# Performance work log

Measured on AMD Instinct MI355X. Metric: run time of the kernel, lower is better.

## Reference

```python
import jax, jax.numpy as jnp
import numpy as np

N_LAYER, N_HEAD, D_MODEL, D_K, D_HIDDEN = 8, 8, 512, 64, 2048
N_CONTEXT, N_DICT, MAG = 1024, 8192, 0.05
B, T = 8, 1024


def _sinusoidal_pos(n_context, d_model):
    i2 = np.arange(0, d_model, 2)
    inv = 1.0 / (10000.0 ** (i2 / d_model))
    ang = np.arange(n_context, dtype=np.float32)[:, None] * inv[None, :]
    pe = np.zeros((1, n_context, d_model), np.float32)
    pe[0, :, 0::2] = np.sin(ang)
    pe[0, :, 1::2] = np.cos(ang)
    return jnp.asarray(pe)


def setup_inputs() -> dict:
    key = jax.random.key(0)
    ks = jax.random.split(key, 10)
    p = lambda k, *s: jax.random.normal(k, s, jnp.float32) * MAG
    return {
        "x": jax.random.randint(ks[0], (B, T), 0, N_DICT),
        "last_only": False,
        "capture_stats": False,
        "embedding": p(ks[1], N_DICT, D_MODEL),
        "pos_embedding": _sinusoidal_pos(N_CONTEXT, D_MODEL),  # fixedpos='True', not trained
        "wq": p(ks[2], N_LAYER, N_HEAD, D_MODEL, D_K),
        "wk": p(ks[3], N_LAYER, N_HEAD, D_MODEL, D_K),
        "wv": p(ks[4], N_LAYER, N_HEAD, D_MODEL, D_MODEL),
        "mlp0": p(ks[5], N_LAYER, D_MODEL, D_HIDDEN),
        "mlpb": p(ks[6], N_LAYER, 1, D_HIDDEN),
        "mlp1": p(ks[7], N_LAYER, D_HIDDEN, D_MODEL),
        "unembedding": p(ks[8], D_MODEL, N_DICT),
        "bias": p(ks[9], 1, 1, N_DICT),
    }


def _ln(x):
    # torch LayerNorm(elementwise_affine=False, bias=False), eps=1e-5, biased var
    mu = jnp.mean(x, axis=-1, keepdims=True)
    var = jnp.mean((x - mu) ** 2, axis=-1, keepdims=True)
    return (x - mu) * jax.lax.rsqrt(var + 1e-5)


def reference(x, last_only, capture_stats, embedding, pos_embedding,
              wq, wk, wv, mlp0, mlpb, mlp1, unembedding, bias):
    del capture_stats  # stats path disabled (capture_stats=False)
    t = x.shape[1]
    h = embedding[x] + pos_embedding[:, :t, :]   # [B,T,M]
    h = _ln(h)                                    # enorm='True', lmul = 1/ldiv = 1
    mask = jnp.tril(jnp.ones((t, t), dtype=bool))

    def layer(h, params):
        wq_l, wk_l, wv_l, m0, mb, m1 = params
        q = jnp.einsum('btm,hmq->bhtq', h, wq_l)
        k = jnp.einsum('bom,hmk->bhok', h, wk_l)
        v = jnp.einsum('bom,hmv->bhov', h, wv_l)
        attn = jnp.einsum('bhtq,bhoq->bhto', q, k)
        # exp(clamp(.,max=50)) then tril then sum-normalize (NOT softmax)
        attn = jnp.where(mask, jnp.exp(jnp.minimum(attn, 50.0)), 0.0)
        attn = attn / (jnp.sum(attn, axis=-1, keepdims=True) + 1e-10)
        vsum = jnp.einsum('bhto,bhov->btv', attn, v)  # sums over heads
        h = _ln(h + vsum)                              # amul = 1, lmul = 1
        y = jax.nn.relu(jnp.einsum('btm,mh->bth', h, m0) + mb)
        y = jnp.einsum('bth,hm->btm', y, m1)
        h = _ln(h + y)                                 # pmul = 1, lmul = 1
        return h, None

    h, _ = jax.lax.scan(layer, h, (wq, wk, wv, mlp0, mlpb, mlp1))
    if last_only:
        h = h[:, -1:, :]
    return jnp.einsum('btm,md->btd', h, unembedding) + bias
```

## Files before the change

kernel.cpp:

```cpp
#include <hip/hip_runtime.h>
#include <hip/hip_bf16.h>

#define BB 8
#define TT 1024
#define DM 512
#define NH 8
#define DK 64
#define DH 2048
#define NL 8
#define ND 8192

typedef __attribute__((ext_vector_type(8))) short short8v;
typedef __attribute__((ext_vector_type(8))) _Float16 f16x8;
typedef __attribute__((ext_vector_type(4))) float f32x4;
typedef __attribute__((ext_vector_type(4))) unsigned short ushort4v;
typedef unsigned short u16;

#define MFMA16(a, b, c) __builtin_amdgcn_mfma_f32_16x16x32_bf16(a, b, c, 0, 0, 0)
#define MFMAH(a, b, c)  __builtin_amdgcn_mfma_f32_16x16x32_f16(a, b, c, 0, 0, 0)

__device__ __forceinline__ u16 bf16_bits(float f) {
  union { __hip_bfloat16 h; u16 u; } cv;
  cv.h = __float2bfloat16(f);
  return cv.u;
}
__device__ __forceinline__ float bits_to_f32(u16 u) {
  union { __hip_bfloat16 h; u16 u; } cv;
  cv.u = u;
  return __bfloat162float(cv.h);
}

__device__ __forceinline__ void gload16(const void* g, void* l) {
  __builtin_amdgcn_global_load_lds(
      (const __attribute__((address_space(1))) unsigned int*)g,
      (__attribute__((address_space(3))) unsigned int*)l, 16, 0, 0);
}

#define WAITVM(N) asm volatile("s_waitcnt vmcnt(" #N ")" ::: "memory")
#define BAR() { __builtin_amdgcn_s_barrier(); asm volatile("" ::: "memory"); }

__device__ __forceinline__ void block_reduce2(float& a, float& b) {
  #pragma unroll
  for (int off = 32; off > 0; off >>= 1) {
    a += __shfl_down(a, off, 64);
    b += __shfl_down(b, off, 64);
  }
  __shared__ float sa[4], sb[4];
  int w = threadIdx.x >> 6;
  if ((threadIdx.x & 63) == 0) { sa[w] = a; sb[w] = b; }
  __syncthreads();
  if (threadIdx.x == 0) {
    sa[0] = sa[0] + sa[1] + sa[2] + sa[3];
    sb[0] = sb[0] + sb[1] + sb[2] + sb[3];
  }
  __syncthreads();
  a = sa[0]; b = sb[0];
}

__device__ __forceinline__ void store_hilo(u16* hh, u16* hl, size_t i, float v) {
  u16 hb = bf16_bits(v);
  hh[i] = hb;
  hl[i] = bf16_bits(v - bits_to_f32(hb));
}

__global__ __launch_bounds__(256) void embed_ln_kernel(
    const int* __restrict__ x, const float* __restrict__ emb,
    const float* __restrict__ pos, float* __restrict__ h,
    u16* __restrict__ hh, u16* __restrict__ hl) {
  int bt = blockIdx.x;
  int t = bt & (TT - 1);
  int tid = threadIdx.x;
  int row = x[bt];
  float v0 = emb[(size_t)row * DM + tid]       + pos[(size_t)t * DM + tid];
  float v1 = emb[(size_t)row * DM + tid + 256] + pos[(size_t)t * DM + tid + 256];
  float s = v0 + v1, sq = v0 * v0 + v1 * v1;
  block_reduce2(s, sq);
  float mu  = s * (1.0f / DM);
  float var = sq * (1.0f / DM) - mu * mu;
  float rs  = rsqrtf(var + 1e-5f);
  float r0 = (v0 - mu) * rs, r1 = (v1 - mu) * rs;
  h[(size_t)bt * DM + tid] = r0;
  h[(size_t)bt * DM + tid + 256] = r1;
  store_hilo(hh, hl, (size_t)bt * DM + tid, r0);
  store_hilo(hh, hl, (size_t)bt * DM + tid + 256, r1);
}

template<bool BF16ADD>
__global__ __launch_bounds__(256) void ln_residual_kernel(
    float* __restrict__ h, const void* __restrict__ add_, int rowStride, int nsum,
    u16* __restrict__ hh, u16* __restrict__ hl) {
  int bt = blockIdx.x;
  int tid = threadIdx.x;
  size_t base = (size_t)bt * (size_t)rowStride;
  float v0 = h[(size_t)bt * DM + tid];
  float v1 = h[(size_t)bt * DM + tid + 256];
  if (BF16ADD) {
    const u16* add = (const u16*)add_;
    for (int i = 0; i < nsum; ++i) {
      v0 += bits_to_f32(add[base + (size_t)i * DM + tid]);
      v1 += bits_to_f32(add[base + (size_t)i * DM + tid + 256]);
    }
  } else {
    const float* add = (const float*)add_;
    for (int i = 0; i < nsum; ++i) {
      v0 += add[base + (size_t)i * DM + tid];
      v1 += add[base + (size_t)i * DM + tid + 256];
    }
  }
  float s = v0 + v1, sq = v0 * v0 + v1 * v1;
  block_reduce2(s, sq);
  float mu  = s * (1.0f / DM);
  float var = sq * (1.0f / DM) - mu * mu;
  float rs  = rsqrtf(var + 1e-5f);
  float r0 = (v0 - mu) * rs, r1 = (v1 - mu) * rs;
  h[(size_t)bt * DM + tid] = r0;
  h[(size_t)bt * DM + tid + 256] = r1;
  store_hilo(hh, hl, (size_t)bt * DM + tid, r0);
  store_hilo(hh, hl, (size_t)bt * DM + tid + 256, r1);
}

__device__ __forceinline__ void tconv_body(
    const float* __restrict__ in, u16* __restrict__ oh, u16* __restrict__ ol,
    int K, int Nb, bool hilo, float (*T)[65]) {
  int tid = threadIdx.x;
  int k0 = blockIdx.x * 64, n0 = blockIdx.y * 64;
  int g = n0 / Nb;
  const float* src = in + (size_t)g * K * Nb + (n0 - g * Nb);
  #pragma unroll
  for (int rep = 0; rep < 16; ++rep) {
    int idx = rep * 256 + tid;
    int i = idx >> 6, j = idx & 63;
    T[i][j] = src[(size_t)(k0 + i) * Nb + j];
  }
  __syncthreads();
  #pragma unroll
  for (int rep = 0; rep < 16; ++rep) {
    int idx = rep * 256 + tid;
    int j = idx >> 6, i = idx & 63;
    float v = T[i][j];
    size_t oa = (size_t)(n0 + j) * K + k0 + i;
    u16 hb = bf16_bits(v);
    oh[oa] = hb;
    if (hilo) ol[oa] = bf16_bits(v - bits_to_f32(hb));
  }
}

__global__ __launch_bounds__(256) void transpose_layer(
    const float* __restrict__ wq, const float* __restrict__ wk,
    const float* __restrict__ wv, const float* __restrict__ w0,
    const float* __restrict__ w1,
    u16* qh, u16* ql, u16* kh, u16* kl, u16* vT, u16* t0, u16* t1) {
  __shared__ float T[64][65];
  int z = blockIdx.z;
  const float* in;
  u16 *oh, *ol = nullptr;
  int K, Nb, gx, gy;
  bool hilo = false;
  switch (z) {
    case 0: in = wq; oh = qh; ol = ql; K = 512;  Nb = 64;   gx = 8;  gy = 8;  hilo = true; break;
    case 1: in = wk; oh = kh; ol = kl; K = 512;  Nb = 64;   gx = 8;  gy = 8;  hilo = true; break;
    case 2: in = wv; oh = vT;          K = 512;  Nb = 512;  gx = 8;  gy = 64; break;
    case 3: in = w0; oh = t0;          K = 512;  Nb = 2048; gx = 8;  gy = 32; break;
    default: in = w1; oh = t1;         K = 2048; Nb = 512;  gx = 32; gy = 8;  break;
  }
  if ((int)blockIdx.x >= gx || (int)blockIdx.y >= gy) return;
  tconv_body(in, oh, ol, K, Nb, hilo, T);
}

__global__ __launch_bounds__(256) void transpose_ue(
    const float* __restrict__ ue, u16* __restrict__ ueT) {
  __shared__ float T[64][65];
  tconv_body(ue, ueT, nullptr, 512, 8192, false, T);
}

template<int MODE>
__global__ __launch_bounds__(256, 2) void gemm_mfma(
    const u16* __restrict__ A, const u16* __restrict__ Bt,
    const float* __restrict__ bias, void* __restrict__ Oo,
    int M, int N, int K) {
  __shared__ u16 As[2][8192];
  __shared__ u16 Bs[2][8192];
  int tid = threadIdx.x;
  int lane = tid & 63, w = tid >> 6;
  int l15 = lane & 15, g = lane >> 4;
  int m0 = blockIdx.x * 128, n0 = blockIdx.y * 128;
  int wr = w >> 1, wc = w & 1;
  int nt = K >> 6;

  f32x4 acc[4][4];
  #pragma unroll
  for (int i = 0; i < 4; ++i)
    #pragma unroll
    for (int j = 0; j < 4; ++j)
      #pragma unroll
      for (int r = 0; r < 4; ++r) acc[i][j][r] = 0.f;

  auto stage = [&](int t, int buf) {
    int k0 = t << 6;
    #pragma unroll
    for (int j = 0; j < 4; ++j) {
      int idx = j * 256 + tid;
      int row = idx >> 3, cs = (idx & 7) ^ (row & 7);
      gload16(A + (size_t)(m0 + row) * K + k0 + cs * 8, &As[buf][idx * 8]);
    }
    #pragma unroll
    for (int j = 0; j < 4; ++j) {
      int idx = j * 256 + tid;
      int row = idx >> 3, cs = (idx & 7) ^ (row & 7);
      gload16(Bt + (size_t)(n0 + row) * K + k0 + cs * 8, &Bs[buf][idx * 8]);
    }
  };

  stage(0, 0);
  for (int t = 0; t < nt; ++t) {
    int cur = t & 1;
    if (t + 1 < nt) {
      stage(t + 1, cur ^ 1);
      WAITVM(8);
    } else {
      WAITVM(0);
    }
    BAR();
    short8v af[4][2], bf[4][2];
    #pragma unroll
    for (int mi = 0; mi < 4; ++mi) {
      int row = wr * 64 + mi * 16 + l15;
      #pragma unroll
      for (int ks = 0; ks < 2; ++ks) {
        int ch = (ks * 4 + g) ^ (row & 7);
        af[mi][ks] = *(const short8v*)&As[cur][row * 64 + ch * 8];
      }
    }
    #pragma unroll
    for (int ni = 0; ni < 4; ++ni) {
      int row = wc * 64 + ni * 16 + l15;
      #pragma unroll
      for (int ks = 0; ks < 2; ++ks) {
        int ch = (ks * 4 + g) ^ (row & 7);
        bf[ni][ks] = *(const short8v*)&Bs[cur][row * 64 + ch * 8];
      }
    }
    #pragma unroll
    for (int mi = 0; mi < 4; ++mi)
      #pragma unroll
      for (int ni = 0; ni < 4; ++ni) {
        acc[mi][ni] = MFMA16(af[mi][0], bf[ni][0], acc[mi][ni]);
        acc[mi][ni] = MFMA16(af[mi][1], bf[ni][1], acc[mi][ni]);
      }
    BAR();
  }

  #pragma unroll
  for (int mi = 0; mi < 4; ++mi) {
    #pragma unroll
    for (int ni = 0; ni < 4; ++ni) {
      int mrow = m0 + wr * 64 + mi * 16 + g * 4;
      int ncol = n0 + wc * 64 + ni * 16 + l15;
      if (MODE == 0) {
        int head = ncol >> 9, dv = ncol & (DM - 1);
        int bb = mrow >> 10, t0 = mrow & (TT - 1);
        ushort4v pk;
        #pragma unroll
        for (int r = 0; r < 4; ++r) pk[r] = bf16_bits(acc[mi][ni][r]);
        *(ushort4v*)((u16*)Oo + ((((size_t)bb * NH + head) * DM + dv) << 10) + t0) = pk;
      } else if (MODE == 1) {
        float bv = bias[ncol];
        #pragma unroll
        for (int r = 0; r < 4; ++r)
          ((u16*)Oo)[(size_t)(mrow + r) * N + ncol] =
              bf16_bits(fmaxf(acc[mi][ni][r] + bv, 0.f));
      } else if (MODE == 2) {
        #pragma unroll
        for (int r = 0; r < 4; ++r)
          ((float*)Oo)[(size_t)(mrow + r) * N + ncol] = acc[mi][ni][r];
      } else {
        float bv = bias[ncol];
        #pragma unroll
        for (int r = 0; r < 4; ++r)
          ((float*)Oo)[(size_t)(mrow + r) * N + ncol] = acc[mi][ni][r] + bv;
      }
    }
  }
}

__global__ __launch_bounds__(256, 2) void gemm_qk(
    const u16* __restrict__ Ah, const u16* __restrict__ Al,
    const u16* __restrict__ Bh, const u16* __restrict__ Bl,
    _Float16* __restrict__ Oq, int K) {
  __shared__ u16 As[2][8192];
  __shared__ u16 Bs[2][8192];
  int tid = threadIdx.x;
  int lane = tid & 63, w = tid >> 6;
  int l15 = lane & 15, g = lane >> 4;
  int m0 = blockIdx.x * 128, n0 = blockIdx.y * 128;
  int wr = w >> 1, wc = w & 1;
  int nt = K >> 5;

  f32x4 acc[4][4];
  #pragma unroll
  for (int i = 0; i < 4; ++i)
    #pragma unroll
    for (int j = 0; j < 4; ++j)
      #pragma unroll
      for (int r = 0; r < 4; ++r) acc[i][j][r] = 0.f;

  auto stage = [&](int t, int buf) {
    int k0 = t << 5;
    #pragma unroll
    for (int j = 0; j < 4; ++j) {
      int idx = j * 256 + tid;
      int row = idx >> 3, cs = (idx & 7) ^ (row & 7);
      const u16* src = (cs < 4) ? Ah : Al;
      gload16(src + (size_t)(m0 + row) * K + k0 + (cs & 3) * 8, &As[buf][idx * 8]);
    }
    #pragma unroll
    for (int j = 0; j < 4; ++j) {
      int idx = j * 256 + tid;
      int row = idx >> 3, cs = (idx & 7) ^ (row & 7);
      const u16* src = (cs < 4) ? Bh : Bl;
      gload16(src + (size_t)(n0 + row) * K + k0 + (cs & 3) * 8, &Bs[buf][idx * 8]);
    }
  };

  stage(0, 0);
  for (int t = 0; t < nt; ++t) {
    int cur = t & 1;
    if (t + 1 < nt) {
      stage(t + 1, cur ^ 1);
      WAITVM(8);
    } else {
      WAITVM(0);
    }
    BAR();
    short8v ah[4], al[4], bh[4], bl[4];
    #pragma unroll
    for (int mi = 0; mi < 4; ++mi) {
      int row = wr * 64 + mi * 16 + l15;
      ah[mi] = *(const short8v*)&As[cur][row * 64 + (g ^ (row & 7)) * 8];
      al[mi] = *(const short8v*)&As[cur][row * 64 + ((g + 4) ^ (row & 7)) * 8];
    }
    #pragma unroll
    for (int ni = 0; ni < 4; ++ni) {
      int row = wc * 64 + ni * 16 + l15;
      bh[ni] = *(const short8v*)&Bs[cur][row * 64 + (g ^ (row & 7)) * 8];
      bl[ni] = *(const short8v*)&Bs[cur][row * 64 + ((g + 4) ^ (row & 7)) * 8];
    }
    #pragma unroll
    for (int mi = 0; mi < 4; ++mi)
      #pragma unroll
      for (int ni = 0; ni < 4; ++ni) {
        acc[mi][ni] = MFMA16(ah[mi], bh[ni], acc[mi][ni]);
        acc[mi][ni] = MFMA16(al[mi], bh[ni], acc[mi][ni]);
        acc[mi][ni] = MFMA16(ah[mi], bl[ni], acc[mi][ni]);
      }
    BAR();
  }

  #pragma unroll
  for (int mi = 0; mi < 4; ++mi) {
    #pragma unroll
    for (int ni = 0; ni < 4; ++ni) {
      int mrow = m0 + wr * 64 + mi * 16 + g * 4;
      int ncol = n0 + wc * 64 + ni * 16 + l15;
      int head = ncol >> 6, dk = ncol & (DK - 1);
      int bb = mrow >> 10;
      #pragma unroll
      for (int r = 0; r < 4; ++r) {
        int t = (mrow + r) & (TT - 1);
        size_t ad = (((size_t)bb * NH + head) * TT + t) * DK + dk;
        Oq[ad] = (_Float16)acc[mi][ni][r];
      }
    }
  }
}

__global__ __launch_bounds__(256, 2) void attn_mfma_kernel(
    const _Float16* __restrict__ qp, const _Float16* __restrict__ kp,
    const __hip_bfloat16* __restrict__ vt_, u16* __restrict__ o) {
  __shared__ __align__(16) u16 Pl[2][64 * 64];
  __shared__ float rs_lds[64];

  const u16* vtp = (const u16*)vt_;

  int tid = threadIdx.x;
  int lane = tid & 63;
  int w = tid >> 6;
  int l15 = lane & 15, g = lane >> 4;
  int blk = blockIdx.x;
  int bh = blk & 63;
  int tt = 15 - (blk >> 6);

  if (tid < 64) rs_lds[tid] = 0.f;

  size_t qbase = (((size_t)bh * TT) + tt * 64 + w * 16 + l15) * DK + g * 8;
  f16x8 qf[2];
  qf[0] = *(const f16x8*)(qp + qbase);
  qf[1] = *(const f16x8*)(qp + qbase + 32);

  f32x4 oacc[4][8];
  #pragma unroll
  for (int qt = 0; qt < 4; ++qt)
    #pragma unroll
    for (int dv = 0; dv < 8; ++dv)
      #pragma unroll
      for (int r = 0; r < 4; ++r) oacc[qt][dv][r] = 0.f;

  __syncthreads();

  for (int ot = 0; ot <= tt; ++ot) {
    int ob = ot * 64;
    bool diag = (ot == tt);
    int buf = ot & 1;
    size_t kbase = (((size_t)bh * TT) + ob + l15) * DK + g * 8;
    f16x8 kf[4][2];
    #pragma unroll
    for (int ct = 0; ct < 4; ++ct) {
      kf[ct][0] = *(const f16x8*)(kp + kbase + (size_t)ct * 16 * DK);
      kf[ct][1] = *(const f16x8*)(kp + kbase + (size_t)ct * 16 * DK + 32);
    }
    f32x4 sacc[4];
    #pragma unroll
    for (int ct = 0; ct < 4; ++ct)
      #pragma unroll
      for (int r = 0; r < 4; ++r) sacc[ct][r] = 0.f;
    #pragma unroll
    for (int ct = 0; ct < 4; ++ct)
      #pragma unroll
      for (int ks = 0; ks < 2; ++ks)
        sacc[ct] = MFMAH(qf[ks], kf[ct][ks], sacc[ct]);
    size_t vbase = ((size_t)bh * DM + w * 128 + l15) * TT + ob + g * 8;
    short8v vf0[8];
    #pragma unroll
    for (int dv = 0; dv < 8; ++dv)
      vf0[dv] = *(const short8v*)(vtp + vbase + (size_t)dv * 16 * TT);
    float psum[4] = {0.f, 0.f, 0.f, 0.f};
    #pragma unroll
    for (int ct = 0; ct < 4; ++ct) {
      #pragma unroll
      for (int r = 0; r < 4; ++r) {
        float s = sacc[ct][r];
        float p = __expf(fminf(s, 50.f));
        if (diag && (ct * 16 + l15 > w * 16 + g * 4 + r)) p = 0.f;
        psum[r] += p;
        int q = w * 16 + g * 4 + r;
        int byte = (q * 128 + (ct * 16 + l15) * 2) ^ ((q & 7) << 4);
        *(u16*)((char*)Pl[buf] + byte) = bf16_bits(p);
      }
    }
    #pragma unroll
    for (int r = 0; r < 4; ++r) {
      float v = psum[r];
      v += __shfl_xor(v, 1, 16);
      v += __shfl_xor(v, 2, 16);
      v += __shfl_xor(v, 4, 16);
      v += __shfl_xor(v, 8, 16);
      if (l15 == 0) rs_lds[w * 16 + g * 4 + r] += v;
    }
    __syncthreads();
    short8v vf1[8];
    #pragma unroll
    for (int dv = 0; dv < 8; ++dv)
      vf1[dv] = *(const short8v*)(vtp + vbase + 32 + (size_t)dv * 16 * TT);
    short8v pf[4];
    #pragma unroll
    for (int qt = 0; qt < 4; ++qt) {
      int q = qt * 16 + l15;
      int byte = (q * 128 + g * 16) ^ ((q & 7) << 4);
      pf[qt] = *(short8v*)((char*)Pl[buf] + byte);
    }
    #pragma unroll
    for (int dv = 0; dv < 8; ++dv)
      #pragma unroll
      for (int qt = 0; qt < 4; ++qt)
        oacc[qt][dv] = MFMA16(pf[qt], vf0[dv], oacc[qt][dv]);
    #pragma unroll
    for (int qt = 0; qt < 4; ++qt) {
      int q = qt * 16 + l15;
      int byte = (q * 128 + 64 + g * 16) ^ ((q & 7) << 4);
      pf[qt] = *(short8v*)((char*)Pl[buf] + byte);
    }
    #pragma unroll
    for (int dv = 0; dv < 8; ++dv)
      #pragma unroll
      for (int qt = 0; qt < 4; ++qt)
        oacc[qt][dv] = MFMA16(pf[qt], vf1[dv], oacc[qt][dv]);
  }
  __syncthreads();
  int b = bh >> 3, hh2 = bh & 7;
  #pragma unroll
  for (int qt = 0; qt < 4; ++qt) {
    #pragma unroll
    for (int r = 0; r < 4; ++r) {
      int q = qt * 16 + g * 4 + r;
      float rs = 1.0f / (rs_lds[q] + 1e-10f);
      size_t rowbase = ((size_t)(b * TT + tt * 64 + q)) * (NH * DM) + hh2 * DM + w * 128 + l15;
      #pragma unroll
      for (int dv = 0; dv < 8; ++dv)
        o[rowbase + dv * 16] = bf16_bits(oacc[qt][dv][r] * rs);
    }
  }
}

extern "C" void kernel_launch(void* const* d_in, const int* in_sizes, int n_in,
                              void* d_out, int out_size, void* d_ws, size_t ws_size,
                              hipStream_t stream) {
  (void)in_sizes; (void)n_in; (void)out_size; (void)ws_size;
  const int*   x   = (const int*)d_in[0];
  const float* emb = (const float*)d_in[3];
  const float* pos = (const float*)d_in[4];
  const float* wq  = (const float*)d_in[5];
  const float* wk  = (const float*)d_in[6];
  const float* wv  = (const float*)d_in[7];
  const float* m0  = (const float*)d_in[8];
  const float* mb  = (const float*)d_in[9];
  const float* m1  = (const float*)d_in[10];
  const float* ue  = (const float*)d_in[11];
  const float* ub  = (const float*)d_in[12];
  float* out = (float*)d_out;
  float* ws  = (float*)d_ws;

  const int M = BB * TT;

  float* h   = ws;
  u16*   hh  = (u16*)(ws + 4194304);
  u16*   hl  = hh + 4194304;
  float* yb  = ws + 8388608;
  u16*   ueT = (u16*)(ws + 12582912);

  u16* outus = (u16*)d_out;
  u16* vt  = outus;
  _Float16* qf16 = (_Float16*)(outus + 33554432);
  _Float16* kf16 = (_Float16*)(outus + 37748736);
  u16* wT  = outus + 41943040;
  u16 *wqTh = wT, *wqTl = wT + 262144, *wkTh = wT + 524288, *wkTl = wT + 786432;
  u16* wvT = wT + 1048576;
  u16* w0T = wT + 3145728;
  u16* w1T = wT + 4194304;
  u16* Ob  = outus + 67108864;
  u16* hid = outus;

  embed_ln_kernel<<<M, 256, 0, stream>>>(x, emb, pos, h, hh, hl);

  for (int l = 0; l < NL; ++l) {
    transpose_layer<<<dim3(32, 64, 5), 256, 0, stream>>>(
        wq + (size_t)l * NH * DM * DK, wk + (size_t)l * NH * DM * DK,
        wv + (size_t)l * NH * DM * DM, m0 + (size_t)l * DM * DH,
        m1 + (size_t)l * DH * DM,
        wqTh, wqTl, wkTh, wkTl, wvT, w0T, w1T);
    gemm_qk<<<dim3(64, 4), 256, 0, stream>>>(hh, hl, wqTh, wqTl, qf16, DM);
    gemm_qk<<<dim3(64, 4), 256, 0, stream>>>(hh, hl, wkTh, wkTl, kf16, DM);
    gemm_mfma<0><<<dim3(64, 32), 256, 0, stream>>>(hh, wvT, nullptr, vt, M, NH * DM, DM);
    attn_mfma_kernel<<<BB * NH * (TT / 64), 256, 0, stream>>>(
        qf16, kf16, (const __hip_bfloat16*)vt, Ob);
    ln_residual_kernel<true><<<M, 256, 0, stream>>>(h, Ob, NH * DM, NH, hh, hl);
    gemm_mfma<1><<<dim3(64, 16), 256, 0, stream>>>(hh, w0T, mb + (size_t)l * DH, hid, M, DH, DM);
    gemm_mfma<2><<<dim3(64, 4), 256, 0, stream>>>(hid, w1T, nullptr, yb, M, DM, DH);
    ln_residual_kernel<false><<<M, 256, 0, stream>>>(h, yb, DM, 1, hh, hl);
  }
  transpose_ue<<<dim3(8, 128), 256, 0, stream>>>(ue, ueT);
  gemm_mfma<3><<<dim3(64, 64), 256, 0, stream>>>(hh, ueT, ub, out, M, ND, DM);
}
```

Baseline: 2.587 ms.

## Use fp16 for Q/K projections, stage K in LDS, add MFMA priority hints

Replaces the split bf16 hi/lo three-MFMA Q/K projection with a single fp16 GEMM, using fp16 copies of activations and weights, which halves the K-loop iterations and drops a third of the MFMAs. The attention kernel now double-buffers K tiles through LDS with async loads instead of direct global reads. It also adds s_setprio around MFMA blocks and flattens the transpose launch grid to avoid idle blocks. fp16 has a narrower exponent range than the hi/lo bf16 scheme, so Q/K precision and range behaviour change, and the scores feed an exp clamped at 50.

Measured after the change: 2.351 ms. 9.1% less time.

```diff
diff --git a/kernel.cpp b/kernel.cpp
--- a/kernel.cpp
+++ b/kernel.cpp
@@ -57,16 +57,10 @@
   a = sa[0]; b = sb[0];
 }
 
-__device__ __forceinline__ void store_hilo(u16* hh, u16* hl, size_t i, float v) {
-  u16 hb = bf16_bits(v);
-  hh[i] = hb;
-  hl[i] = bf16_bits(v - bits_to_f32(hb));
-}
-
 __global__ __launch_bounds__(256) void embed_ln_kernel(
     const int* __restrict__ x, const float* __restrict__ emb,
     const float* __restrict__ pos, float* __restrict__ h,
-    u16* __restrict__ hh, u16* __restrict__ hl) {
+    u16* __restrict__ hh, _Float16* __restrict__ hf) {
   int bt = blockIdx.x;
   int t = bt & (TT - 1);
   int tid = threadIdx.x;
@@ -81,14 +75,16 @@
   float r0 = (v0 - mu) * rs, r1 = (v1 - mu) * rs;
   h[(size_t)bt * DM + tid] = r0;
   h[(size_t)bt * DM + tid + 256] = r1;
-  store_hilo(hh, hl, (size_t)bt * DM + tid, r0);
-  store_hilo(hh, hl, (size_t)bt * DM + tid + 256, r1);
+  hh[(size_t)bt * DM + tid] = bf16_bits(r0);
+  hh[(size_t)bt * DM + tid + 256] = bf16_bits(r1);
+  hf[(size_t)bt * DM + tid] = (_Float16)r0;
+  hf[(size_t)bt * DM + tid + 256] = (_Float16)r1;
 }
 
 template<bool BF16ADD>
 __global__ __launch_bounds__(256) void ln_residual_kernel(
     float* __restrict__ h, const void* __restrict__ add_, int rowStride, int nsum,
-    u16* __restrict__ hh, u16* __restrict__ hl) {
+    u16* __restrict__ hh, _Float16* __restrict__ hf) {
   int bt = blockIdx.x;
   int tid = threadIdx.x;
   size_t base = (size_t)bt * (size_t)rowStride;
@@ -115,17 +111,34 @@
   float r0 = (v0 - mu) * rs, r1 = (v1 - mu) * rs;
   h[(size_t)bt * DM + tid] = r0;
   h[(size_t)bt * DM + tid + 256] = r1;
-  store_hilo(hh, hl, (size_t)bt * DM + tid, r0);
-  store_hilo(hh, hl, (size_t)bt * DM + tid + 256, r1);
-}
-
-__device__ __forceinline__ void tconv_body(
-    const float* __restrict__ in, u16* __restrict__ oh, u16* __restrict__ ol,
-    int K, int Nb, bool hilo, float (*T)[65]) {
-  int tid = threadIdx.x;
-  int k0 = blockIdx.x * 64, n0 = blockIdx.y * 64;
+  hh[(size_t)bt * DM + tid] = bf16_bits(r0);
+  hh[(size_t)bt * DM + tid + 256] = bf16_bits(r1);
+  hf[(size_t)bt * DM + tid] = (_Float16)r0;
+  hf[(size_t)bt * DM + tid + 256] = (_Float16)r1;
+}
+
+__global__ __launch_bounds__(256) void transpose_layer(
+    const float* __restrict__ wq, const float* __restrict__ wk,
+    const float* __restrict__ wv, const float* __restrict__ w0,
+    const float* __restrict__ w1,
+    _Float16* __restrict__ qT, _Float16* __restrict__ kT,
+    u16* __restrict__ vT, u16* __restrict__ t0, u16* __restrict__ t1) {
+  __shared__ float T[64][65];
+  int t = blockIdx.x;
+  const float* in;
+  _Float16* of = nullptr;
+  u16* ob = nullptr;
+  int K, Nb;
+  if (t < 64)       { in = wq; of = qT; K = 512;  Nb = 64; }
+  else if (t < 128) { in = wk; of = kT; K = 512;  Nb = 64;   t -= 64; }
+  else if (t < 640) { in = wv; ob = vT; K = 512;  Nb = 512;  t -= 128; }
+  else if (t < 896) { in = w0; ob = t0; K = 512;  Nb = 2048; t -= 640; }
+  else              { in = w1; ob = t1; K = 2048; Nb = 512;  t -= 896; }
+  int ntx = K >> 6;
+  int k0 = (t % ntx) * 64, n0 = (t / ntx) * 64;
   int g = n0 / Nb;
   const float* src = in + (size_t)g * K * Nb + (n0 - g * Nb);
+  int tid = threadIdx.x;
   #pragma unroll
   for (int rep = 0; rep < 16; ++rep) {
     int idx = rep * 256 + tid;
@@ -139,38 +152,29 @@
     int j = idx >> 6, i = idx & 63;
     float v = T[i][j];
     size_t oa = (size_t)(n0 + j) * K + k0 + i;
-    u16 hb = bf16_bits(v);
-    oh[oa] = hb;
-    if (hilo) ol[oa] = bf16_bits(v - bits_to_f32(hb));
-  }
-}
-
-__global__ __launch_bounds__(256) void transpose_layer(
-    const float* __restrict__ wq, const float* __restrict__ wk,
-    const float* __restrict__ wv, const float* __restrict__ w0,
-    const float* __restrict__ w1,
-    u16* qh, u16* ql, u16* kh, u16* kl, u16* vT, u16* t0, u16* t1) {
-  __shared__ float T[64][65];
-  int z = blockIdx.z;
-  const float* in;
-  u16 *oh, *ol = nullptr;
-  int K, Nb, gx, gy;
-  bool hilo = false;
-  switch (z) {
-    case 0: in = wq; oh = qh; ol = ql; K = 512;  Nb = 64;   gx = 8;  gy = 8;  hilo = true; break;
-    case 1: in = wk; oh = kh; ol = kl; K = 512;  Nb = 64;   gx = 8;  gy = 8;  hilo = true; break;
-    case 2: in = wv; oh = vT;          K = 512;  Nb = 512;  gx = 8;  gy = 64; break;
-    case 3: in = w0; oh = t0;          K = 512;  Nb = 2048; gx = 8;  gy = 32; break;
-    default: in = w1; oh = t1;         K = 2048; Nb = 512;  gx = 32; gy = 8;  break;
-  }
-  if ((int)blockIdx.x >= gx || (int)blockIdx.y >= gy) return;
-  tconv_body(in, oh, ol, K, Nb, hilo, T);
+    if (of) of[oa] = (_Float16)v;
+    else    ob[oa] = bf16_bits(v);
+  }
 }
 
 __global__ __launch_bounds__(256) void transpose_ue(
     const float* __restrict__ ue, u16* __restrict__ ueT) {
   __shared__ float T[64][65];
-  tconv_body(ue, ueT, nullptr, 512, 8192, false, T);
+  int tid = threadIdx.x;
+  int k0 = blockIdx.x * 64, n0 = blockIdx.y * 64;
+  #pragma unroll
+  for (int rep = 0; rep < 16; ++rep) {
+    int idx = rep * 256 + tid;
+    int i = idx >> 6, j = idx & 63;
+    T[i][j] = ue[(size_t)(k0 + i) * ND + n0 + j];
+  }
+  __syncthreads();
+  #pragma unroll
+  for (int rep = 0; rep < 16; ++rep) {
+    int idx = rep * 256 + tid;
+    int j = idx >> 6, i = idx & 63;
+    ueT[(size_t)(n0 + j) * DM + k0 + i] = bf16_bits(T[i][j]);
+  }
 }
 
 template<int MODE>
@@ -240,6 +244,7 @@
         bf[ni][ks] = *(const short8v*)&Bs[cur][row * 64 + ch * 8];
       }
     }
+    __builtin_amdgcn_s_setprio(1);
     #pragma unroll
     for (int mi = 0; mi < 4; ++mi)
       #pragma unroll
@@ -247,6 +252,7 @@
         acc[mi][ni] = MFMA16(af[mi][0], bf[ni][0], acc[mi][ni]);
         acc[mi][ni] = MFMA16(af[mi][1], bf[ni][1], acc[mi][ni]);
       }
+    __builtin_amdgcn_s_setprio(0);
     BAR();
   }
 
@@ -283,18 +289,17 @@
   }
 }
 
-__global__ __launch_bounds__(256, 2) void gemm_qk(
-    const u16* __restrict__ Ah, const u16* __restrict__ Al,
-    const u16* __restrict__ Bh, const u16* __restrict__ Bl,
+__global__ __launch_bounds__(256, 2) void gemm_qk_f16(
+    const _Float16* __restrict__ A, const _Float16* __restrict__ Bt,
     _Float16* __restrict__ Oq, int K) {
-  __shared__ u16 As[2][8192];
-  __shared__ u16 Bs[2][8192];
+  __shared__ _Float16 As[2][8192];
+  __shared__ _Float16 Bs[2][8192];
   int tid = threadIdx.x;
   int lane = tid & 63, w = tid >> 6;
   int l15 = lane & 15, g = lane >> 4;
   int m0 = blockIdx.x * 128, n0 = blockIdx.y * 128;
   int wr = w >> 1, wc = w & 1;
-  int nt = K >> 5;
+  int nt = K >> 6;
 
   f32x4 acc[4][4];
   #pragma unroll
@@ -305,20 +310,18 @@
       for (int r = 0; r < 4; ++r) acc[i][j][r] = 0.f;
 
   auto stage = [&](int t, int buf) {
-    int k0 = t << 5;
+    int k0 = t << 6;
     #pragma unroll
     for (int j = 0; j < 4; ++j) {
       int idx = j * 256 + tid;
       int row = idx >> 3, cs = (idx & 7) ^ (row & 7);
-      const u16* src = (cs < 4) ? Ah : Al;
-      gload16(src + (size_t)(m0 + row) * K + k0 + (cs & 3) * 8, &As[buf][idx * 8]);
+      gload16(A + (size_t)(m0 + row) * K + k0 + cs * 8, &As[buf][idx * 8]);
     }
     #pragma unroll
     for (int j = 0; j < 4; ++j) {
       int idx = j * 256 + tid;
       int row = idx >> 3, cs = (idx & 7) ^ (row & 7);
-      const u16* src = (cs < 4) ? Bh : Bl;
-      gload16(src + (size_t)(n0 + row) * K + k0 + (cs & 3) * 8, &Bs[buf][idx * 8]);
+      gload16(Bt + (size_t)(n0 + row) * K + k0 + cs * 8, &Bs[buf][idx * 8]);
     }
   };
 
@@ -332,27 +335,34 @@
       WAITVM(0);
     }
     BAR();
-    short8v ah[4], al[4], bh[4], bl[4];
+    f16x8 af[4][2], bf[4][2];
     #pragma unroll
     for (int mi = 0; mi < 4; ++mi) {
       int row = wr * 64 + mi * 16 + l15;
-      ah[mi] = *(const short8v*)&As[cur][row * 64 + (g ^ (row & 7)) * 8];
-      al[mi] = *(const short8v*)&As[cur][row * 64 + ((g + 4) ^ (row & 7)) * 8];
+      #pragma unroll
+      for (int ks = 0; ks < 2; ++ks) {
+        int ch = (ks * 4 + g) ^ (row & 7);
+        af[mi][ks] = *(const f16x8*)&As[cur][row * 64 + ch * 8];
+      }
     }
     #pragma unroll
     for (int ni = 0; ni < 4; ++ni) {
       int row = wc * 64 + ni * 16 + l15;
-      bh[ni] = *(const short8v*)&Bs[cur][row * 64 + (g ^ (row & 7)) * 8];
-      bl[ni] = *(const short8v*)&Bs[cur][row * 64 + ((g + 4) ^ (row & 7)) * 8];
-    }
+      #pragma unroll
+      for (int ks = 0; ks < 2; ++ks) {
+        int ch = (ks * 4 + g) ^ (row & 7);
+        bf[ni][ks] = *(const f16x8*)&Bs[cur][row * 64 + ch * 8];
+      }
+    }
+    __builtin_amdgcn_s_setprio(1);
     #pragma unroll
     for (int mi = 0; mi < 4; ++mi)
       #pragma unroll
       for (int ni = 0; ni < 4; ++ni) {
-        acc[mi][ni] = MFMA16(ah[mi], bh[ni], acc[mi][ni]);
-        acc[mi][ni] = MFMA16(al[mi], bh[ni], acc[mi][ni]);
-        acc[mi][ni] = MFMA16(ah[mi], bl[ni], acc[mi][ni]);
-      }
+        acc[mi][ni] = MFMAH(af[mi][0], bf[ni][0], acc[mi][ni]);
+        acc[mi][ni] = MFMAH(af[mi][1], bf[ni][1], acc[mi][ni]);
+      }
+    __builtin_amdgcn_s_setprio(0);
     BAR();
   }
 
@@ -367,8 +377,7 @@
       #pragma unroll
       for (int r = 0; r < 4; ++r) {
         int t = (mrow + r) & (TT - 1);
-        size_t ad = (((size_t)bb * NH + head) * TT + t) * DK + dk;
-        Oq[ad] = (_Float16)acc[mi][ni][r];
+        Oq[(((size_t)bb * NH + head) * TT + t) * DK + dk] = (_Float16)acc[mi][ni][r];
       }
     }
   }
@@ -378,10 +387,10 @@
     const _Float16* __restrict__ qp, const _Float16* __restrict__ kp,
     const __hip_bfloat16* __restrict__ vt_, u16* __restrict__ o) {
   __shared__ __align__(16) u16 Pl[2][64 * 64];
+  __shared__ __align__(16) _Float16 Kl[2][64 * 64];
   __shared__ float rs_lds[64];
 
   const u16* vtp = (const u16*)vt_;
-
   int tid = threadIdx.x;
   int lane = tid & 63;
   int w = tid >> 6;
@@ -392,6 +401,16 @@
 
   if (tid < 64) rs_lds[tid] = 0.f;
 
+  auto stageK = [&](int ot, int buf) {
+    int ob = ot * 64;
+    #pragma unroll
+    for (int j = 0; j < 2; ++j) {
+      int idx = j * 256 + tid;
+      int row = idx >> 3, cs = (idx & 7) ^ (row & 7);
+      gload16(kp + ((size_t)bh * TT + ob + row) * DK + cs * 8, &Kl[buf][idx * 8]);
+    }
+  };
+
   size_t qbase = (((size_t)bh * TT) + tt * 64 + w * 16 + l15) * DK + g * 8;
   f16x8 qf[2];
   qf[0] = *(const f16x8*)(qp + qbase);
@@ -405,29 +424,30 @@
       #pragma unroll
       for (int r = 0; r < 4; ++r) oacc[qt][dv][r] = 0.f;
 
+  stageK(0, 0);
+  WAITVM(0);
   __syncthreads();
 
   for (int ot = 0; ot <= tt; ++ot) {
     int ob = ot * 64;
     bool diag = (ot == tt);
     int buf = ot & 1;
-    size_t kbase = (((size_t)bh * TT) + ob + l15) * DK + g * 8;
-    f16x8 kf[4][2];
+    if (ot < tt) stageK(ot + 1, buf ^ 1);
+    f32x4 sacc[4];
+    #pragma unroll
+    for (int ct = 0; ct < 4; ++ct)
+      #pragma unroll
+      for (int r = 0; r < 4; ++r) sacc[ct][r] = 0.f;
+    __builtin_amdgcn_s_setprio(1);
     #pragma unroll
     for (int ct = 0; ct < 4; ++ct) {
-      kf[ct][0] = *(const f16x8*)(kp + kbase + (size_t)ct * 16 * DK);
-      kf[ct][1] = *(const f16x8*)(kp + kbase + (size_t)ct * 16 * DK + 32);
-    }
-    f32x4 sacc[4];
-    #pragma unroll
-    for (int ct = 0; ct < 4; ++ct)
-      #pragma unroll
-      for (int r = 0; r < 4; ++r) sacc[ct][r] = 0.f;
-    #pragma unroll
-    for (int ct = 0; ct < 4; ++ct)
-      #pragma unroll
-      for (int ks = 0; ks < 2; ++ks)
-        sacc[ct] = MFMAH(qf[ks], kf[ct][ks], sacc[ct]);
+      int row = ct * 16 + l15;
+      f16x8 k0 = *(const f16x8*)&Kl[buf][row * 64 + ((g) ^ (row & 7)) * 8];
+      f16x8 k1 = *(const f16x8*)&Kl[buf][row * 64 + ((4 + g) ^ (row & 7)) * 8];
+      sacc[ct] = MFMAH(qf[0], k0, sacc[ct]);
+      sacc[ct] = MFMAH(qf[1], k1, sacc[ct]);
+    }
+    __builtin_amdgcn_s_setprio(0);
     size_t vbase = ((size_t)bh * DM + w * 128 + l15) * TT + ob + g * 8;
     short8v vf0[8];
     #pragma unroll
@@ -456,7 +476,8 @@
       v += __shfl_xor(v, 8, 16);
       if (l15 == 0) rs_lds[w * 16 + g * 4 + r] += v;
     }
-    __syncthreads();
+    WAITVM(0);
+    BAR();
     short8v vf1[8];
     #pragma unroll
     for (int dv = 0; dv < 8; ++dv)
@@ -468,22 +489,26 @@
       int byte = (q * 128 + g * 16) ^ ((q & 7) << 4);
       pf[qt] = *(short8v*)((char*)Pl[buf] + byte);
     }
+    __builtin_amdgcn_s_setprio(1);
     #pragma unroll
     for (int dv = 0; dv < 8; ++dv)
       #pragma unroll
       for (int qt = 0; qt < 4; ++qt)
         oacc[qt][dv] = MFMA16(pf[qt], vf0[dv], oacc[qt][dv]);
+    __builtin_amdgcn_s_setprio(0);
     #pragma unroll
     for (int qt = 0; qt < 4; ++qt) {
       int q = qt * 16 + l15;
       int byte = (q * 128 + 64 + g * 16) ^ ((q & 7) << 4);
       pf[qt] = *(short8v*)((char*)Pl[buf] + byte);
     }
+    __builtin_amdgcn_s_setprio(1);
     #pragma unroll
     for (int dv = 0; dv < 8; ++dv)
       #pragma unroll
       for (int qt = 0; qt < 4; ++qt)
         oacc[qt][dv] = MFMA16(pf[qt], vf1[dv], oacc[qt][dv]);
+    __builtin_amdgcn_s_setprio(0);
   }
   __syncthreads();
   int b = bh >> 3, hh2 = bh & 7;
@@ -521,41 +546,42 @@
 
   const int M = BB * TT;
 
-  float* h   = ws;
-  u16*   hh  = (u16*)(ws + 4194304);
-  u16*   hl  = hh + 4194304;
-  float* yb  = ws + 8388608;
-  u16*   ueT = (u16*)(ws + 12582912);
+  float*    h    = ws;
+  u16*      hh   = (u16*)(ws + 4194304);
+  _Float16* hf16 = (_Float16*)(ws + 6291456);
+  float*    yb   = ws + 8388608;
+  u16*      ueT  = (u16*)(ws + 12582912);
 
   u16* outus = (u16*)d_out;
-  u16* vt  = outus;
+  u16* vt = outus;
   _Float16* qf16 = (_Float16*)(outus + 33554432);
   _Float16* kf16 = (_Float16*)(outus + 37748736);
-  u16* wT  = outus + 41943040;
-  u16 *wqTh = wT, *wqTl = wT + 262144, *wkTh = wT + 524288, *wkTl = wT + 786432;
-  u16* wvT = wT + 1048576;
-  u16* w0T = wT + 3145728;
-  u16* w1T = wT + 4194304;
+  u16* wT = outus + 41943040;
+  _Float16* wqT = (_Float16*)wT;
+  _Float16* wkT = (_Float16*)(wT + 262144);
+  u16* wvT = wT + 524288;
+  u16* w0T = wT + 2621440;
+  u16* w1T = wT + 3670016;
   u16* Ob  = outus + 67108864;
   u16* hid = outus;
 
-  embed_ln_kernel<<<M, 256, 0, stream>>>(x, emb, pos, h, hh, hl);
+  embed_ln_kernel<<<M, 256, 0, stream>>>(x, emb, pos, h, hh, hf16);
 
   for (int l = 0; l < NL; ++l) {
-    transpose_layer<<<dim3(32, 64, 5), 256, 0, stream>>>(
+    transpose_layer<<<1152, 256, 0, stream>>>(
         wq + (size_t)l * NH * DM * DK, wk + (size_t)l * NH * DM * DK,
         wv + (size_t)l * NH * DM * DM, m0 + (size_t)l * DM * DH,
         m1 + (size_t)l * DH * DM,
-        wqTh, wqTl, wkTh, wkTl, wvT, w0T, w1T);
-    gemm_qk<<<dim3(64, 4), 256, 0, stream>>>(hh, hl, wqTh, wqTl, qf16, DM);
-    gemm_qk<<<dim3(64, 4), 256, 0, stream>>>(hh, hl, wkTh, wkTl, kf16, DM);
+        wqT, wkT, wvT, w0T, w1T);
+    gemm_qk_f16<<<dim3(64, 4), 256, 0, stream>>>(hf16, wqT, qf16, DM);
+    gemm_qk_f16<<<dim3(64, 4), 256, 0, stream>>>(hf16, wkT, kf16, DM);
     gemm_mfma<0><<<dim3(64, 32), 256, 0, stream>>>(hh, wvT, nullptr, vt, M, NH * DM, DM);
     attn_mfma_kernel<<<BB * NH * (TT / 64), 256, 0, stream>>>(
         qf16, kf16, (const __hip_bfloat16*)vt, Ob);
-    ln_residual_kernel<true><<<M, 256, 0, stream>>>(h, Ob, NH * DM, NH, hh, hl);
+    ln_residual_kernel<true><<<M, 256, 0, stream>>>(h, Ob, NH * DM, NH, hh, hf16);
     gemm_mfma<1><<<dim3(64, 16), 256, 0, stream>>>(hh, w0T, mb + (size_t)l * DH, hid, M, DH, DM);
     gemm_mfma<2><<<dim3(64, 4), 256, 0, stream>>>(hid, w1T, nullptr, yb, M, DM, DH);
-    ln_residual_kernel<false><<<M, 256, 0, stream>>>(h, yb, DM, 1, hh, hl);
+    ln_residual_kernel<false><<<M, 256, 0, stream>>>(h, yb, DM, 1, hh, hf16);
   }
   transpose_ue<<<dim3(8, 128), 256, 0, stream>>>(ue, ueT);
   gemm_mfma<3><<<dim3(64, 64), 256, 0, stream>>>(hh, ueT, ub, out, M, ND, DM);
```
